# Kernel tuning notes

Hardware: AMD Instinct MI355X
Metric: run time of the kernel (lower is better)

Reference implementation:

```python
import jax, jax.numpy as jnp
import numpy as np

B, C, H, W = 8, 512, 64, 64
NH = 8                 # num_heads
HD = C // NH           # head_dim = 64
WIN = 8 * 8            # tokens per window
NW = (H * W) // WIN    # number of windows = 64


def setup_inputs() -> dict:
    key = jax.random.key(0)
    ks = jax.random.split(key, 8)
    w = lambda k, shape: jax.random.normal(k, shape, jnp.float32) * 0.02
    return {
        "x": jax.random.normal(ks[0], (B, C, H, W), jnp.float32),
        "Wq": w(ks[1], (C, C)), "bq": jnp.zeros((C,), jnp.float32),
        "Wk": w(ks[2], (C, C)), "bk": jnp.zeros((C,), jnp.float32),
        "Wv": w(ks[3], (C, C)), "bv": jnp.zeros((C,), jnp.float32),
        "Bbias": w(ks[4], (WIN, WIN)),  # additive relative bias per (q,k) position in window
    }


def reference(x, Wq, bq, Wk, bk, Wv, bv, Bbias):
    shape = x.shape
    # (B, C, H, W) -> (B, n_windows, window, C)
    xw = x.reshape(shape[0], NW, WIN, C)
    # QKV projections (torch Linear: y = x @ W^T + b)
    q = (xw @ Wq.T + bq).reshape(B, NW, WIN, NH, HD).transpose(0, 1, 3, 2, 4)
    k = (xw @ Wk.T + bk).reshape(B, NW, WIN, NH, HD).transpose(0, 1, 3, 2, 4)
    v = (xw @ Wv.T + bv).reshape(B, NW, WIN, NH, HD).transpose(0, 1, 3, 2, 4)
    scale = 1.0 / jnp.sqrt(jnp.float32(HD))
    scores = jnp.einsum("bwhqd,bwhkd->bwhqk", q, k) * scale + Bbias  # bias broadcasts over b,w,h
    probs = jax.nn.softmax(scores, axis=-1)
    out = jnp.einsum("bwhqk,bwhkd->bwhqd", probs, v)
    out = out.transpose(0, 1, 3, 2, 4).reshape(shape)
    return out
```

## Files before the change

### kernel.cpp

```cpp
#include <hip/hip_runtime.h>
#include <hip/hip_bf16.h>


typedef __attribute__((ext_vector_type(8))) short bf16x8;
typedef __attribute__((ext_vector_type(4))) float f32x4;

#define GLDS(gp, lp) __builtin_amdgcn_global_load_lds( \
    (const __attribute__((address_space(1))) unsigned int*)(gp), \
    (__attribute__((address_space(3))) unsigned int*)(lp), 16, 0, 0)

__device__ __forceinline__ unsigned short f2bf(float f) {
  union { float f; unsigned int u; } v; v.f = f;
  unsigned int r = v.u + 0x7fffu + ((v.u >> 16) & 1u);
  return (unsigned short)(r >> 16);
}

__global__ __launch_bounds__(256) void prep_convert(
    const float* __restrict__ X, const float* __restrict__ Wq,
    const float* __restrict__ Wk, const float* __restrict__ Wv,
    unsigned short* __restrict__ Xb, unsigned short* __restrict__ Wc) {
  const unsigned int i = blockIdx.x * 256 + threadIdx.x;
  const float* src;
  unsigned short* dst;
  if (i < 2097152u) {
    src = X + (size_t)i * 8;
    dst = Xb + (size_t)i * 8;
  } else {
    const unsigned int j = i - 2097152u;
    const unsigned int e = j * 8;
    const unsigned int n = e >> 9, kk = e & 511;
    src = ((n < 512) ? Wq : (n < 1024 ? Wk : Wv)) + (size_t)(n & 511) * 512 + kk;
    dst = Wc + (size_t)n * 512 + kk;
  }
  float4 f0 = *(const float4*)(src);
  float4 f1 = *(const float4*)(src + 4);
  __align__(16) unsigned short u[8];
  u[0] = f2bf(f0.x); u[1] = f2bf(f0.y); u[2] = f2bf(f0.z); u[3] = f2bf(f0.w);
  u[4] = f2bf(f1.x); u[5] = f2bf(f1.y); u[6] = f2bf(f1.z); u[7] = f2bf(f1.w);
  *(bf16x8*)(dst) = *(const bf16x8*)(u);
}

__global__ __launch_bounds__(512, 2) void qkv_gemm_256(
    const unsigned short* __restrict__ Xb, const unsigned short* __restrict__ Wc,
    const float* __restrict__ bq, const float* __restrict__ bk,
    const float* __restrict__ bv,
    unsigned short* __restrict__ Qo, unsigned short* __restrict__ Ko,
    unsigned short* __restrict__ Vo) {
  __shared__ __align__(16) char LDS[131072];

  const int tid  = threadIdx.x;
  const int lane = tid & 63;
  const int wid  = tid >> 6;
  const int wm = wid >> 2, wn = wid & 3;

  const int work = (int)(blockIdx.x & 7) * 96 + (int)(blockIdx.x >> 3);
  const int bx = work % 6, by = work / 6;
  const int n0 = bx * 256, m0 = by * 256;

  const int lcol  = ((lane & 3) * 8) ^ ((lane >= 32) ? 16 : 0);
  const int arow0 = (wid >> 1) * 16 + (lane >> 2);
  const int acol0 = (wid & 1) * 32 + lcol;

#define STAGE_A(half, tt) do { \
    const unsigned short* g = Xb + (size_t)(m0 + (half) * 128 + arow0) * 512 + (tt) * 64 + acol0; \
    char* l = LDS + ((tt) & 1) * 32768 + (half) * 16384 + wid * 1024; \
    GLDS(g, l); \
    GLDS(g + 64 * 512, l + 8192); \
  } while (0)

#define STAGE_B(half, tt) do { \
    const unsigned short* g = Wc + (size_t)(n0 + (half) * 128 + arow0) * 512 + (tt) * 64 + acol0; \
    char* l = LDS + 65536 + ((tt) & 1) * 32768 + (half) * 16384 + wid * 1024; \
    GLDS(g, l); \
    GLDS(g + 64 * 512, l + 8192); \
  } while (0)

  const int sloff = (((lane & 15) * 64) + ((lane >> 4) * 16)) ^ ((lane & 8) ? 32 : 0);
  char* const Ab = LDS + wm * 16384 + sloff;
  char* const Bb2 = LDS + 65536 + (wn >> 1) * 16384 + sloff;
  const int bfr = (wn & 1) * 4;

  f32x4 acc[8][4];
#pragma unroll
  for (int i = 0; i < 8; ++i)
#pragma unroll
    for (int j = 0; j < 4; ++j) acc[i][j] = (f32x4){0.f, 0.f, 0.f, 0.f};

#define LDA(mh, bo) do { \
    _Pragma("unroll") for (int mi = 0; mi < 4; ++mi) \
    _Pragma("unroll") for (int ks = 0; ks < 2; ++ks) \
      a[mi][ks] = *(const bf16x8*)(Ab + (bo) + ((mh) * 4 + mi) * 2048 + ks * 1024); \
  } while (0)

#define LDB(dst, nh, bo) do { \
    _Pragma("unroll") for (int ni = 0; ni < 2; ++ni) \
    _Pragma("unroll") for (int ks = 0; ks < 2; ++ks) \
      dst[ni][ks] = *(const bf16x8*)(Bb2 + (bo) + (bfr + (nh) * 2 + ni) * 2048 + ks * 1024); \
  } while (0)

#define MM(mh, nh, bb) do { \
    _Pragma("unroll") for (int mi = 0; mi < 4; ++mi) \
    _Pragma("unroll") for (int ni = 0; ni < 2; ++ni) \
    _Pragma("unroll") for (int ks = 0; ks < 2; ++ks) \
      acc[(mh) * 4 + mi][(nh) * 2 + ni] = __builtin_amdgcn_mfma_f32_16x16x32_bf16( \
          a[mi][ks], bb[ni][ks], acc[(mh) * 4 + mi][(nh) * 2 + ni], 0, 0, 0); \
  } while (0)

  STAGE_A(0, 0); STAGE_A(1, 0); STAGE_B(0, 0); STAGE_B(1, 0);
  asm volatile("s_waitcnt vmcnt(0)" ::: "memory");
  __builtin_amdgcn_s_barrier();

  for (int t = 0; t < 8; ++t) {
    const int bo = (t & 1) * 32768;
    if (t + 1 < 8) {
      STAGE_A(0, t + 1); STAGE_A(1, t + 1);
      STAGE_B(0, t + 1); STAGE_B(1, t + 1);
    }
    {
      bf16x8 a[4][2], b0[2][2], b1[2][2];
      LDA(0, bo); LDB(b0, 0, bo);
      MM(0, 0, b0);
      LDB(b1, 1, bo);
      MM(0, 1, b1);
      LDA(1, bo);
      MM(1, 1, b1);
      MM(1, 0, b0);
    }
    if (t + 1 < 8) asm volatile("s_waitcnt vmcnt(0)" ::: "memory");
    __builtin_amdgcn_s_barrier();
  }

  {
    const int p = n0 >> 9;
    const float* bias = (p == 0) ? bq : (p == 1) ? bk : bv;
    const float qs = (p == 0) ? 0.125f : 1.0f;
    const int hi = lane >> 4, lr = lane & 15;
    const int h = ((n0 & 511) + wn * 64) >> 6;
    char* const scr = LDS + wid * 8192;
    float bsv[4];
#pragma unroll
    for (int ni = 0; ni < 4; ++ni)
      bsv[ni] = bias[(n0 & 511) + wn * 64 + ni * 16 + lr];

#pragma unroll
    for (int wh = 0; wh < 2; ++wh) {
      asm volatile("s_waitcnt lgkmcnt(0)" ::: "memory");
      __builtin_amdgcn_sched_barrier(0);
      if (p < 2) {
#pragma unroll
        for (int f = 0; f < 4; ++f)
#pragma unroll
          for (int ni = 0; ni < 4; ++ni) {
            const int d = ni * 16 + lr;
#pragma unroll
            for (int rr = 0; rr < 4; ++rr) {
              const int t = f * 16 + hi * 4 + rr;
              const int off = t * 64 + (d ^ ((t & 7) << 3));
              *(unsigned short*)(scr + off * 2) =
                  f2bf((acc[wh * 4 + f][ni][rr] + bsv[ni]) * qs);
            }
          }
      } else {
#pragma unroll
        for (int f = 0; f < 4; ++f)
#pragma unroll
          for (int ni = 0; ni < 4; ++ni) {
            const int d = ni * 16 + lr;
            const int t0 = f * 16 + hi * 4;
            ushort4 pk;
            pk.x = f2bf(acc[wh * 4 + f][ni][0] + bsv[ni]);
            pk.y = f2bf(acc[wh * 4 + f][ni][1] + bsv[ni]);
            pk.z = f2bf(acc[wh * 4 + f][ni][2] + bsv[ni]);
            pk.w = f2bf(acc[wh * 4 + f][ni][3] + bsv[ni]);
            const int off = d * 64 + (t0 ^ ((d & 7) << 3));
            *(ushort4*)(scr + off * 2) = pk;
          }
      }
      asm volatile("s_waitcnt lgkmcnt(0)" ::: "memory");
      __builtin_amdgcn_sched_barrier(0);
      const int win = (m0 + wm * 128 + wh * 64) >> 6;
      unsigned short* dst =
          ((p == 0) ? Qo : (p == 1) ? Ko : Vo) + (size_t)(win * 8 + h) * 4096;
#pragma unroll
      for (int i = 0; i < 8; ++i) {
        const int r = i * 8 + (lane >> 3);
        const int c = lane & 7;
        const int off = r * 64 + ((c ^ (r & 7)) * 8);
        bf16x8 row = *(const bf16x8*)(scr + off * 2);
        *(bf16x8*)(dst + r * 64 + c * 8) = row;
      }
    }
  }
#undef STAGE_A
#undef STAGE_B
#undef LDA
#undef LDB
#undef MM
}

__global__ __launch_bounds__(64) void attn_win(
    const unsigned short* __restrict__ Qp, const unsigned short* __restrict__ Kp,
    const unsigned short* __restrict__ Vp, const float* __restrict__ Bb,
    float* __restrict__ out) {
  __shared__ __align__(16) unsigned short P[64 * 72];
  const int lane = threadIdx.x;
  const int win = blockIdx.x >> 3;
  const int h   = blockIdx.x & 7;
  const size_t base = (size_t)(win * 8 + h) * 4096;
  const unsigned short* q = Qp + base;
  const unsigned short* k = Kp + base;
  const unsigned short* v = Vp + base;
  const int lr = lane & 15;
  const int hi = lane >> 4;

  bf16x8 qa[4][2], kb[4][2];
#pragma unroll
  for (int mt = 0; mt < 4; ++mt)
#pragma unroll
    for (int ks = 0; ks < 2; ++ks)
      qa[mt][ks] = *(const bf16x8*)(q + (size_t)(mt * 16 + lr) * 64 + ks * 32 + hi * 8);
#pragma unroll
  for (int nt = 0; nt < 4; ++nt)
#pragma unroll
    for (int ks = 0; ks < 2; ++ks)
      kb[nt][ks] = *(const bf16x8*)(k + (size_t)(nt * 16 + lr) * 64 + ks * 32 + hi * 8);

  f32x4 s[4][4];
#pragma unroll
  for (int mt = 0; mt < 4; ++mt)
#pragma unroll
    for (int nt = 0; nt < 4; ++nt) {
      s[mt][nt] = (f32x4){0.f, 0.f, 0.f, 0.f};
      s[mt][nt] = __builtin_amdgcn_mfma_f32_16x16x32_bf16(qa[mt][0], kb[nt][0], s[mt][nt], 0, 0, 0);
      s[mt][nt] = __builtin_amdgcn_mfma_f32_16x16x32_bf16(qa[mt][1], kb[nt][1], s[mt][nt], 0, 0, 0);
    }

#pragma unroll
  for (int mt = 0; mt < 4; ++mt)
#pragma unroll
    for (int nt = 0; nt < 4; ++nt)
#pragma unroll
      for (int rr = 0; rr < 4; ++rr)
        s[mt][nt][rr] += Bb[(mt * 16 + hi * 4 + rr) * 64 + nt * 16 + lr];

  float inv[4][4];
#pragma unroll
  for (int mt = 0; mt < 4; ++mt)
#pragma unroll
    for (int rr = 0; rr < 4; ++rr) {
      float m = fmaxf(fmaxf(s[mt][0][rr], s[mt][1][rr]),
                      fmaxf(s[mt][2][rr], s[mt][3][rr]));
      m = fmaxf(m, __shfl_xor(m, 1));
      m = fmaxf(m, __shfl_xor(m, 2));
      m = fmaxf(m, __shfl_xor(m, 4));
      m = fmaxf(m, __shfl_xor(m, 8));
      float sum = 0.f;
#pragma unroll
      for (int nt = 0; nt < 4; ++nt) {
        float e = __expf(s[mt][nt][rr] - m);
        s[mt][nt][rr] = e;
        sum += e;
      }
      sum += __shfl_xor(sum, 1);
      sum += __shfl_xor(sum, 2);
      sum += __shfl_xor(sum, 4);
      sum += __shfl_xor(sum, 8);
      inv[mt][rr] = 1.0f / sum;
    }

#pragma unroll
  for (int mt = 0; mt < 4; ++mt)
#pragma unroll
    for (int nt = 0; nt < 4; ++nt)
#pragma unroll
      for (int rr = 0; rr < 4; ++rr)
        P[(mt * 16 + hi * 4 + rr) * 72 + nt * 16 + lr] =
            f2bf(s[mt][nt][rr] * inv[mt][rr]);
  __syncthreads();

  bf16x8 pa[4][2], vb[4][2];
#pragma unroll
  for (int mt = 0; mt < 4; ++mt)
#pragma unroll
    for (int ks = 0; ks < 2; ++ks)
      pa[mt][ks] = *(const bf16x8*)(&P[(mt * 16 + lr) * 72 + ks * 32 + hi * 8]);
#pragma unroll
  for (int nt = 0; nt < 4; ++nt)
#pragma unroll
    for (int ks = 0; ks < 2; ++ks)
      vb[nt][ks] = *(const bf16x8*)(v + (size_t)(nt * 16 + lr) * 64 + ks * 32 + hi * 8);

  f32x4 o[4][4];
#pragma unroll
  for (int mt = 0; mt < 4; ++mt)
#pragma unroll
    for (int nt = 0; nt < 4; ++nt) {
      o[mt][nt] = (f32x4){0.f, 0.f, 0.f, 0.f};
      o[mt][nt] = __builtin_amdgcn_mfma_f32_16x16x32_bf16(pa[mt][0], vb[nt][0], o[mt][nt], 0, 0, 0);
      o[mt][nt] = __builtin_amdgcn_mfma_f32_16x16x32_bf16(pa[mt][1], vb[nt][1], o[mt][nt], 0, 0, 0);
    }

  float* op = out + (size_t)win * 32768 + h * 64;
#pragma unroll
  for (int mt = 0; mt < 4; ++mt)
#pragma unroll
    for (int nt = 0; nt < 4; ++nt)
#pragma unroll
      for (int rr = 0; rr < 4; ++rr)
        op[(size_t)(mt * 16 + hi * 4 + rr) * 512 + nt * 16 + lr] = o[mt][nt][rr];
}

extern "C" void kernel_launch(void* const* d_in, const int* in_sizes, int n_in,
                              void* d_out, int out_size, void* d_ws, size_t ws_size,
                              hipStream_t stream) {
  const float* x     = (const float*)d_in[0];
  const float* Wq    = (const float*)d_in[1];
  const float* bq    = (const float*)d_in[2];
  const float* Wk    = (const float*)d_in[3];
  const float* bk    = (const float*)d_in[4];
  const float* Wv    = (const float*)d_in[5];
  const float* bv    = (const float*)d_in[6];
  const float* Bbias = (const float*)d_in[7];
  float* out = (float*)d_out;

  unsigned short* Wc = (unsigned short*)d_ws;
  unsigned short* Xb = (unsigned short*)((char*)d_ws + ((size_t)2 << 20));
  unsigned short* Q  = (unsigned short*)((char*)d_ws + ((size_t)36 << 20));
  unsigned short* K  = (unsigned short*)((char*)d_ws + ((size_t)68 << 20));
  unsigned short* V  = (unsigned short*)((char*)d_ws + ((size_t)100 << 20));

  prep_convert<<<dim3(8576), dim3(256), 0, stream>>>(x, Wq, Wk, Wv, Xb, Wc);
  qkv_gemm_256<<<dim3(768), dim3(512), 0, stream>>>(Xb, Wc, bq, bk, bv, Q, K, V);
  attn_win<<<dim3(4096), dim3(64), 0, stream>>>(Q, K, V, Bbias, out);
}
```

Measured before the change: 111.6 us.

## Shrink QKV GEMM tile from 256x256 to 128x128 with higher occupancy

Rewrites the QKV projection GEMM to use 128x128 output tiles per 512-thread block instead of 256x256. Each wave now holds a 32x64 accumulator, LDS use drops to 64KB, and launch bounds request 4 blocks per CU. The grid grows to 3072 blocks to improve load balance and latency hiding. The epilogue is reworked so each wave writes half a window's Q/K rows or V-transposed columns. The trade is less operand reuse per block, which means more global and LDS traffic per FLOP.

```diff
diff --git a/kernel.cpp b/kernel.cpp
--- a/kernel.cpp
+++ b/kernel.cpp
@@ -40,91 +40,78 @@
   *(bf16x8*)(dst) = *(const bf16x8*)(u);
 }
 
-__global__ __launch_bounds__(512, 2) void qkv_gemm_256(
+__global__ __launch_bounds__(512, 4) void qkv_gemm_128(
     const unsigned short* __restrict__ Xb, const unsigned short* __restrict__ Wc,
     const float* __restrict__ bq, const float* __restrict__ bk,
     const float* __restrict__ bv,
     unsigned short* __restrict__ Qo, unsigned short* __restrict__ Ko,
     unsigned short* __restrict__ Vo) {
-  __shared__ __align__(16) char LDS[131072];
+  __shared__ __align__(16) char LDS[65536];
 
   const int tid  = threadIdx.x;
   const int lane = tid & 63;
   const int wid  = tid >> 6;
-  const int wm = wid >> 2, wn = wid & 3;
-
-  const int work = (int)(blockIdx.x & 7) * 96 + (int)(blockIdx.x >> 3);
-  const int bx = work % 6, by = work / 6;
-  const int n0 = bx * 256, m0 = by * 256;
+  const int wm = wid >> 1, wn = wid & 1;
+
+  const int work = (int)(blockIdx.x & 7) * 384 + (int)(blockIdx.x >> 3);
+  const int bx = work % 12, by = work / 12;
+  const int n0 = bx * 128, m0 = by * 128;
 
   const int lcol  = ((lane & 3) * 8) ^ ((lane >= 32) ? 16 : 0);
   const int arow0 = (wid >> 1) * 16 + (lane >> 2);
   const int acol0 = (wid & 1) * 32 + lcol;
 
-#define STAGE_A(half, tt) do { \
-    const unsigned short* g = Xb + (size_t)(m0 + (half) * 128 + arow0) * 512 + (tt) * 64 + acol0; \
-    char* l = LDS + ((tt) & 1) * 32768 + (half) * 16384 + wid * 1024; \
+#define STAGE_A(tt) do { \
+    const unsigned short* g = Xb + (size_t)(m0 + arow0) * 512 + (tt) * 64 + acol0; \
+    char* l = LDS + ((tt) & 1) * 16384 + wid * 1024; \
     GLDS(g, l); \
     GLDS(g + 64 * 512, l + 8192); \
   } while (0)
 
-#define STAGE_B(half, tt) do { \
-    const unsigned short* g = Wc + (size_t)(n0 + (half) * 128 + arow0) * 512 + (tt) * 64 + acol0; \
-    char* l = LDS + 65536 + ((tt) & 1) * 32768 + (half) * 16384 + wid * 1024; \
+#define STAGE_B(tt) do { \
+    const unsigned short* g = Wc + (size_t)(n0 + arow0) * 512 + (tt) * 64 + acol0; \
+    char* l = LDS + 32768 + ((tt) & 1) * 16384 + wid * 1024; \
     GLDS(g, l); \
     GLDS(g + 64 * 512, l + 8192); \
   } while (0)
 
   const int sloff = (((lane & 15) * 64) + ((lane >> 4) * 16)) ^ ((lane & 8) ? 32 : 0);
-  char* const Ab = LDS + wm * 16384 + sloff;
-  char* const Bb2 = LDS + 65536 + (wn >> 1) * 16384 + sloff;
-  const int bfr = (wn & 1) * 4;
-
-  f32x4 acc[8][4];
-#pragma unroll
-  for (int i = 0; i < 8; ++i)
+  char* const Ab = LDS + sloff;
+  char* const Bb2 = LDS + 32768 + sloff;
+
+  f32x4 acc[2][4];
+#pragma unroll
+  for (int i = 0; i < 2; ++i)
 #pragma unroll
     for (int j = 0; j < 4; ++j) acc[i][j] = (f32x4){0.f, 0.f, 0.f, 0.f};
 
-#define LDA(mh, bo) do { \
-    _Pragma("unroll") for (int mi = 0; mi < 4; ++mi) \
-    _Pragma("unroll") for (int ks = 0; ks < 2; ++ks) \
-      a[mi][ks] = *(const bf16x8*)(Ab + (bo) + ((mh) * 4 + mi) * 2048 + ks * 1024); \
-  } while (0)
-
-#define LDB(dst, nh, bo) do { \
-    _Pragma("unroll") for (int ni = 0; ni < 2; ++ni) \
-    _Pragma("unroll") for (int ks = 0; ks < 2; ++ks) \
-      dst[ni][ks] = *(const bf16x8*)(Bb2 + (bo) + (bfr + (nh) * 2 + ni) * 2048 + ks * 1024); \
-  } while (0)
-
-#define MM(mh, nh, bb) do { \
-    _Pragma("unroll") for (int mi = 0; mi < 4; ++mi) \
-    _Pragma("unroll") for (int ni = 0; ni < 2; ++ni) \
-    _Pragma("unroll") for (int ks = 0; ks < 2; ++ks) \
-      acc[(mh) * 4 + mi][(nh) * 2 + ni] = __builtin_amdgcn_mfma_f32_16x16x32_bf16( \
-          a[mi][ks], bb[ni][ks], acc[(mh) * 4 + mi][(nh) * 2 + ni], 0, 0, 0); \
-  } while (0)
-
-  STAGE_A(0, 0); STAGE_A(1, 0); STAGE_B(0, 0); STAGE_B(1, 0);
+  STAGE_A(0); STAGE_B(0);
   asm volatile("s_waitcnt vmcnt(0)" ::: "memory");
   __builtin_amdgcn_s_barrier();
 
   for (int t = 0; t < 8; ++t) {
-    const int bo = (t & 1) * 32768;
-    if (t + 1 < 8) {
-      STAGE_A(0, t + 1); STAGE_A(1, t + 1);
-      STAGE_B(0, t + 1); STAGE_B(1, t + 1);
-    }
+    const int bo = (t & 1) * 16384;
+    if (t + 1 < 8) { STAGE_A(t + 1); STAGE_B(t + 1); }
     {
-      bf16x8 a[4][2], b0[2][2], b1[2][2];
-      LDA(0, bo); LDB(b0, 0, bo);
-      MM(0, 0, b0);
-      LDB(b1, 1, bo);
-      MM(0, 1, b1);
-      LDA(1, bo);
-      MM(1, 1, b1);
-      MM(1, 0, b0);
+      bf16x8 a[2][2], b[4][2];
+#pragma unroll
+      for (int mi = 0; mi < 2; ++mi)
+#pragma unroll
+        for (int ks = 0; ks < 2; ++ks)
+          a[mi][ks] = *(const bf16x8*)(Ab + bo + (wm * 2 + mi) * 2048 + ks * 1024);
+#pragma unroll
+      for (int ni = 0; ni < 4; ++ni)
+#pragma unroll
+        for (int ks = 0; ks < 2; ++ks)
+          b[ni][ks] = *(const bf16x8*)(Bb2 + bo + (wn * 4 + ni) * 2048 + ks * 1024);
+#pragma unroll
+      for (int mi = 0; mi < 2; ++mi)
+#pragma unroll
+        for (int ni = 0; ni < 4; ++ni)
+#pragma unroll
+          for (int ks = 0; ks < 2; ++ks)
+            acc[mi][ni] = __builtin_amdgcn_mfma_f32_16x16x32_bf16(
+                a[mi][ks], b[ni][ks], acc[mi][ni], 0, 0, 0);
     }
     if (t + 1 < 8) asm volatile("s_waitcnt vmcnt(0)" ::: "memory");
     __builtin_amdgcn_s_barrier();
@@ -135,67 +122,74 @@
     const float* bias = (p == 0) ? bq : (p == 1) ? bk : bv;
     const float qs = (p == 0) ? 0.125f : 1.0f;
     const int hi = lane >> 4, lr = lane & 15;
-    const int h = ((n0 & 511) + wn * 64) >> 6;
-    char* const scr = LDS + wid * 8192;
+    const int h = ((n0 & 511) >> 6) + wn;
+    const int r0 = m0 + wm * 32;
+    const int win = r0 >> 6;
+    const int tw0 = r0 & 63;
+    char* const scr = LDS + wid * 4096;
     float bsv[4];
 #pragma unroll
     for (int ni = 0; ni < 4; ++ni)
       bsv[ni] = bias[(n0 & 511) + wn * 64 + ni * 16 + lr];
 
-#pragma unroll
-    for (int wh = 0; wh < 2; ++wh) {
-      asm volatile("s_waitcnt lgkmcnt(0)" ::: "memory");
-      __builtin_amdgcn_sched_barrier(0);
-      if (p < 2) {
-#pragma unroll
-        for (int f = 0; f < 4; ++f)
-#pragma unroll
-          for (int ni = 0; ni < 4; ++ni) {
-            const int d = ni * 16 + lr;
-#pragma unroll
-            for (int rr = 0; rr < 4; ++rr) {
-              const int t = f * 16 + hi * 4 + rr;
-              const int off = t * 64 + (d ^ ((t & 7) << 3));
-              *(unsigned short*)(scr + off * 2) =
-                  f2bf((acc[wh * 4 + f][ni][rr] + bsv[ni]) * qs);
-            }
+    asm volatile("s_waitcnt lgkmcnt(0)" ::: "memory");
+    __builtin_amdgcn_sched_barrier(0);
+    if (p < 2) {
+#pragma unroll
+      for (int mi = 0; mi < 2; ++mi)
+#pragma unroll
+        for (int ni = 0; ni < 4; ++ni) {
+          const int d = ni * 16 + lr;
+#pragma unroll
+          for (int rr = 0; rr < 4; ++rr) {
+            const int tp = mi * 16 + hi * 4 + rr;
+            const int off = tp * 64 + (d ^ ((tp & 7) << 3));
+            *(unsigned short*)(scr + off * 2) =
+                f2bf((acc[mi][ni][rr] + bsv[ni]) * qs);
           }
-      } else {
-#pragma unroll
-        for (int f = 0; f < 4; ++f)
-#pragma unroll
-          for (int ni = 0; ni < 4; ++ni) {
-            const int d = ni * 16 + lr;
-            const int t0 = f * 16 + hi * 4;
-            ushort4 pk;
-            pk.x = f2bf(acc[wh * 4 + f][ni][0] + bsv[ni]);
-            pk.y = f2bf(acc[wh * 4 + f][ni][1] + bsv[ni]);
-            pk.z = f2bf(acc[wh * 4 + f][ni][2] + bsv[ni]);
-            pk.w = f2bf(acc[wh * 4 + f][ni][3] + bsv[ni]);
-            const int off = d * 64 + (t0 ^ ((d & 7) << 3));
-            *(ushort4*)(scr + off * 2) = pk;
-          }
-      }
-      asm volatile("s_waitcnt lgkmcnt(0)" ::: "memory");
-      __builtin_amdgcn_sched_barrier(0);
-      const int win = (m0 + wm * 128 + wh * 64) >> 6;
-      unsigned short* dst =
-          ((p == 0) ? Qo : (p == 1) ? Ko : Vo) + (size_t)(win * 8 + h) * 4096;
-#pragma unroll
-      for (int i = 0; i < 8; ++i) {
+        }
+    } else {
+#pragma unroll
+      for (int mi = 0; mi < 2; ++mi)
+#pragma unroll
+        for (int ni = 0; ni < 4; ++ni) {
+          const int d = ni * 16 + lr;
+          const int t0p = mi * 16 + hi * 4;
+          ushort4 pk;
+          pk.x = f2bf(acc[mi][ni][0] + bsv[ni]);
+          pk.y = f2bf(acc[mi][ni][1] + bsv[ni]);
+          pk.z = f2bf(acc[mi][ni][2] + bsv[ni]);
+          pk.w = f2bf(acc[mi][ni][3] + bsv[ni]);
+          const int off = d * 32 + (t0p ^ ((d & 3) << 3));
+          *(ushort4*)(scr + off * 2) = pk;
+        }
+    }
+    asm volatile("s_waitcnt lgkmcnt(0)" ::: "memory");
+    __builtin_amdgcn_sched_barrier(0);
+    unsigned short* dst =
+        ((p == 0) ? Qo : (p == 1) ? Ko : Vo) + (size_t)(win * 8 + h) * 4096;
+    if (p < 2) {
+#pragma unroll
+      for (int i = 0; i < 4; ++i) {
         const int r = i * 8 + (lane >> 3);
         const int c = lane & 7;
         const int off = r * 64 + ((c ^ (r & 7)) * 8);
         bf16x8 row = *(const bf16x8*)(scr + off * 2);
-        *(bf16x8*)(dst + r * 64 + c * 8) = row;
+        *(bf16x8*)(dst + (size_t)(tw0 + r) * 64 + c * 8) = row;
+      }
+    } else {
+#pragma unroll
+      for (int i = 0; i < 4; ++i) {
+        const int d = i * 16 + (lane >> 2);
+        const int tc = (lane & 3) * 8;
+        const int off = d * 32 + (tc ^ ((d & 3) << 3));
+        bf16x8 row = *(const bf16x8*)(scr + off * 2);
+        *(bf16x8*)(dst + (size_t)d * 64 + tw0 + tc) = row;
       }
     }
   }
 #undef STAGE_A
 #undef STAGE_B
-#undef LDA
-#undef LDB
-#undef MM
 }
 
 __global__ __launch_bounds__(64) void attn_win(
@@ -330,6 +324,6 @@
   unsigned short* V  = (unsigned short*)((char*)d_ws + ((size_t)100 << 20));
 
   prep_convert<<<dim3(8576), dim3(256), 0, stream>>>(x, Wq, Wk, Wv, Xb, Wc);
-  qkv_gemm_256<<<dim3(768), dim3(512), 0, stream>>>(Xb, Wc, bq, bk, bv, Q, K, V);
+  qkv_gemm_128<<<dim3(3072), dim3(512), 0, stream>>>(Xb, Wc, bq, bk, bv, Q, K, V);
   attn_win<<<dim3(4096), dim3(64), 0, stream>>>(Q, K, V, Bbias, out);
 }
```

After: 115.9 us. 1.04x slower.
